# Performance work log

Hardware: AMD Instinct MI355X
Metric: run time of the kernel (lower is better)

The kernel has to match this reference:

```python
import jax, jax.numpy as jnp
import numpy as np

N, D, H, C = 4096, 4096, 256, 16
NNZ_ATTR, E, NNZ_JM, NNZ_JA = 262144, 131072, 400000, 80000


def setup_inputs() -> dict:
    key = jax.random.key(0)
    ks = jax.random.split(key, 8)
    return {
        "attr_row": jax.random.randint(ks[0], (NNZ_ATTR,), 0, N),
        "attr_col": jax.random.randint(ks[1], (NNZ_ATTR,), 0, D),
        "edge_idx": jax.random.randint(ks[2], (2, E), 0, N),
        "j_mask_idx": jax.random.randint(ks[3], (2, NNZ_JM), 0, N),
        "jaug_mask_idx": jax.random.randint(ks[4], (2, NNZ_JA), 0, N),
        "lin1_w": jax.random.normal(ks[5], (H, D), dtype=jnp.float32) * (1.0 / np.sqrt(D)),
        "lin2_w": jax.random.normal(ks[6], (C, H), dtype=jnp.float32) * (1.0 / np.sqrt(H)),
        "bias2": jax.random.normal(ks[7], (C,), dtype=jnp.float32) * 0.01,
        "n": N,
        "d": D,
    }


def _gcn_norm_dense(a, n):
    # add remaining self loops (binary adjacency -> set diagonal to 1)
    idx = jnp.arange(n)
    a = a.at[idx, idx].set(1.0)
    # PyG gcn_norm: deg = scatter_add(weight, col) = column sums
    deg = a.sum(axis=0)
    dinv = jnp.where(deg > 0, jax.lax.rsqrt(deg), 0.0)
    # out[i] = sum_j dinv[i]*dinv[j]*A[j,i]*x[j]  ->  An = Dinv @ A^T @ Dinv
    return (dinv[:, None] * a.T) * dinv[None, :]


def reference(attr_row, attr_col, edge_idx, j_mask_idx, jaug_mask_idx,
              lin1_w, lin2_w, bias2, n, d):
    # --- edge augmentation: (edges AND J_mask) OR JAug_mask ---
    a = jnp.zeros((n, n), jnp.float32).at[edge_idx[0], edge_idx[1]].set(1.0)
    jm = jnp.zeros((n, n), bool).at[j_mask_idx[0], j_mask_idx[1]].set(True)
    ja = jnp.zeros((n, n), bool).at[jaug_mask_idx[0], jaug_mask_idx[1]].set(True)
    a_aug = jnp.maximum(jnp.where(jm, a, 0.0), ja.astype(jnp.float32))

    # --- layer 1: spmm(sparse binary X, W1^T), gcn_norm, propagate (no bias) ---
    x = jnp.zeros((n, d), jnp.float32).at[attr_row, attr_col].add(1.0)
    h = x @ lin1_w.T                     # [n, H]
    an = _gcn_norm_dense(a_aug, n)       # [n, n] normalized adjacency
    h = jax.nn.relu(an @ h)              # propagate + relu
    # dropout is identity in eval mode

    # --- layer 2: standard GCNConv with bias ---
    h2 = h @ lin2_w.T                    # [n, C]
    out = an @ h2 + bias2
    return out
```

## Files before the change

kernel.cpp:

```cpp
#include <hip/hip_runtime.h>

#define N_      4096
#define D_      4096
#define H_      256
#define C_      16
#define NNZ_ATTR 262144
#define E_      131072
#define NNZ_JM  400000
#define NNZ_JA  80000
#define WORDS   128
#define ADJ_STRIDE 128
#define ASTR    128
#define NT      256

#define OFF_EBT  ((size_t)0)
#define OFF_ABT  ((size_t)(2u<<20))
#define OFF_CNT  ((size_t)(4u<<20))
#define OFF_DINV (OFF_CNT + (size_t)(16u<<10))
#define OFF_DEG  (OFF_CNT + (size_t)(32u<<10))
#define OFF_CCOL (OFF_CNT + (size_t)(48u<<10))
#define OFF_ADJ  (OFF_CCOL + (size_t)(2u<<20))
#define OFF_W1T  (OFF_ADJ + (size_t)(2u<<20))
#define OFF_H1   (OFF_W1T + (size_t)(4u<<20))
#define OFF_H2   (OFF_H1  + (size_t)(4u<<20))

#define ZERO_BYTES (OFF_CNT + (size_t)(16u<<10))
#define ZB_BLOCKS  1028

#define SB_ATTR  0
#define SB_EDGE  1024
#define SB_JA    1536
#define SB_DIAG  1849
#define SB_TR    1865
#define SB_TOTAL 2889

__global__ void k_zero(uint4* __restrict__ zp) {
    zp[(size_t)blockIdx.x * NT + threadIdx.x] = make_uint4(0u, 0u, 0u, 0u);
}

__global__ void k_scat1(const int* __restrict__ attr_row, const int* __restrict__ attr_col,
                        const int* __restrict__ edge, const int* __restrict__ jaug,
                        const float* __restrict__ w1,
                        unsigned* __restrict__ ebt, unsigned* __restrict__ abt,
                        unsigned* __restrict__ cnt, unsigned* __restrict__ ccol,
                        float* __restrict__ w1t) {
    __shared__ float tile[32][33];
    const int b = blockIdx.x, t = threadIdx.x;
    if (b < SB_EDGE) {
        int i = b * NT + t;
        int r = attr_row[i];
        unsigned pos = atomicAdd(&cnt[r], 1u);
        if (pos < ASTR) ccol[(size_t)r * ASTR + pos] = (unsigned)attr_col[i];
    } else if (b < SB_JA) {
        int j = (b - SB_EDGE) * NT + t;
        int p = edge[j], q = edge[E_ + j];
        atomicOr(&ebt[(size_t)q * WORDS + (p >> 5)], 1u << (p & 31));
    } else if (b < SB_DIAG) {
        int j = (b - SB_JA) * NT + t;
        if (j < NNZ_JA) {
            int p = jaug[j], q = jaug[NNZ_JA + j];
            atomicOr(&abt[(size_t)q * WORDS + (p >> 5)], 1u << (p & 31));
        }
    } else if (b < SB_TR) {
        int r = (b - SB_DIAG) * NT + t;
        atomicOr(&abt[(size_t)r * WORDS + (r >> 5)], 1u << (r & 31));
    } else {
        int bb = b - SB_TR;
        int gx = bb & 127, gy = bb >> 7;
        int tx = t & 31, ty = t >> 5;
        int col = gx * 32 + tx;
        #pragma unroll
        for (int j = 0; j < 4; ++j)
            tile[ty + j * 8][tx] = w1[(size_t)(gy * 32 + ty + j * 8) * D_ + col];
        __syncthreads();
        int ocol = gy * 32 + tx;
        #pragma unroll
        for (int j = 0; j < 4; ++j)
            w1t[(size_t)(gx * 32 + ty + j * 8) * H_ + ocol] = tile[tx][ty + j * 8];
    }
}

__global__ void k_scat2(const int* __restrict__ jmsk,
                        const unsigned* __restrict__ ebt, unsigned* __restrict__ abt) {
    int i = blockIdx.x * NT + threadIdx.x;
    if (i >= NNZ_JM) return;
    int p = jmsk[i], q = jmsk[NNZ_JM + i];
    size_t w = (size_t)q * WORDS + (p >> 5);
    if ((ebt[w] >> (p & 31)) & 1u)
        atomicOr(&abt[w], 1u << (p & 31));
}

__global__ void k_rowh1(const unsigned* __restrict__ abt, const unsigned* __restrict__ cnt,
                        const unsigned* __restrict__ ccol, const float* __restrict__ w1t,
                        float* __restrict__ dinv, int* __restrict__ deg,
                        int* __restrict__ adj, float* __restrict__ h1s) {
    __shared__ __align__(16) char smem[4640];
    unsigned* cols = (unsigned*)smem;
    float* part = (float*)(smem + 512);
    float* sdinv = (float*)(smem + 512 + 4096);
    const int b = blockIdx.x, t = threadIdx.x;
    int wv = t >> 6, lane = t & 63;
    int q = 4 * b + wv;
    {
        uint2 m2 = ((const uint2*)(abt + (size_t)q * WORDS))[lane];
        unsigned w0 = m2.x, w1b = m2.y;
        int c = __popc(w0) + __popc(w1b);
        int pre = c;
        #pragma unroll
        for (int d2 = 1; d2 < 64; d2 <<= 1) {
            int x = __shfl_up(pre, d2);
            if (lane >= d2) pre += x;
        }
        int excl = pre - c;
        int total = __shfl(pre, 63);
        if (lane == 0) {
            float dv = rsqrtf((float)total);
            dinv[q] = dv;
            sdinv[wv] = dv;
            deg[q] = total < ADJ_STRIDE ? total : ADJ_STRIDE;
        }
        unsigned idx = (unsigned)excl;
        int* arow = adj + (size_t)q * ADJ_STRIDE;
        int base0 = lane * 64;
        while (w0)  { int bp = __ffs(w0) - 1;  w0  &= w0 - 1;  if (idx < ADJ_STRIDE) arow[idx] = base0 + bp;      ++idx; }
        while (w1b) { int bp = __ffs(w1b) - 1; w1b &= w1b - 1; if (idx < ADJ_STRIDE) arow[idx] = base0 + 32 + bp; ++idx; }
    }
    __syncthreads();
    int g = t >> 6;
    for (int i = 0; i < 4; ++i) {
        int r = 4 * b + i;
        unsigned m = min(cnt[r], (unsigned)ASTR);
        if ((unsigned)t < m) cols[t] = ccol[(size_t)r * ASTR + t];
        __syncthreads();
        float4 acc = make_float4(0.f, 0.f, 0.f, 0.f);
        unsigned j = (unsigned)g;
        for (; j + 12 < m; j += 16) {
            unsigned c0 = cols[j], c1 = cols[j + 4], c2 = cols[j + 8], c3 = cols[j + 12];
            float4 v0 = *(const float4*)&w1t[(size_t)c0 * H_ + lane * 4];
            float4 v1 = *(const float4*)&w1t[(size_t)c1 * H_ + lane * 4];
            float4 v2 = *(const float4*)&w1t[(size_t)c2 * H_ + lane * 4];
            float4 v3 = *(const float4*)&w1t[(size_t)c3 * H_ + lane * 4];
            acc.x += v0.x + v1.x + v2.x + v3.x;
            acc.y += v0.y + v1.y + v2.y + v3.y;
            acc.z += v0.z + v1.z + v2.z + v3.z;
            acc.w += v0.w + v1.w + v2.w + v3.w;
        }
        for (; j < m; j += 4) {
            unsigned c0 = cols[j];
            float4 v0 = *(const float4*)&w1t[(size_t)c0 * H_ + lane * 4];
            acc.x += v0.x; acc.y += v0.y; acc.z += v0.z; acc.w += v0.w;
        }
        ((float4*)part)[g * 64 + lane] = acc;
        __syncthreads();
        int comp = t & 3, idx4 = t >> 2;
        float s0 = part[(0 * 64 + idx4) * 4 + comp];
        float s1 = part[(1 * 64 + idx4) * 4 + comp];
        float s2 = part[(2 * 64 + idx4) * 4 + comp];
        float s3 = part[(3 * 64 + idx4) * 4 + comp];
        h1s[(size_t)r * H_ + t] = (s0 + s1 + s2 + s3) * sdinv[i];
        __syncthreads();
    }
}

__global__ void k_prop1(const int* __restrict__ adj, const int* __restrict__ deg,
                        const float* __restrict__ dinv, const float* __restrict__ h1s,
                        const float* __restrict__ w2, float* __restrict__ h2s) {
    __shared__ __align__(16) char smem[2688];
    int* adj_s = (int*)smem;
    float* hrow = (float*)(smem + 512);
    float* partial = (float*)(smem + 512 + 1024);
    const int b = blockIdx.x, t = threadIdx.x;
    int c = t & 15, g = t >> 4;
    float w2r[16];
    #pragma unroll
    for (int kk = 0; kk < 16; ++kk) w2r[kk] = w2[(size_t)c * H_ + g * 16 + kk];
    for (int i = 0; i < 4; ++i) {
        int q = 4 * b + i;
        __syncthreads();
        if (t < ADJ_STRIDE) adj_s[t] = adj[(size_t)q * ADJ_STRIDE + t];
        __syncthreads();
        int dg = deg[q];
        float acc = 0.f;
        int j = 0;
        for (; j + 4 <= dg; j += 4) {
            int p0 = adj_s[j], p1 = adj_s[j + 1], p2 = adj_s[j + 2], p3 = adj_s[j + 3];
            acc += h1s[(size_t)p0 * H_ + t] + h1s[(size_t)p1 * H_ + t]
                 + h1s[(size_t)p2 * H_ + t] + h1s[(size_t)p3 * H_ + t];
        }
        for (; j < dg; ++j) acc += h1s[(size_t)adj_s[j] * H_ + t];
        float dq = dinv[q];
        hrow[t] = fmaxf(acc * dq, 0.f);
        __syncthreads();
        float part = 0.f;
        #pragma unroll
        for (int kk = 0; kk < 16; ++kk) part += hrow[g * 16 + kk] * w2r[kk];
        partial[g * 17 + c] = part;
        __syncthreads();
        if (t < 16) {
            float s = 0.f;
            #pragma unroll
            for (int g2 = 0; g2 < 16; ++g2) s += partial[g2 * 17 + t];
            h2s[(size_t)q * C_ + t] = s * dq;
        }
    }
}

__global__ void k_prop2(const int* __restrict__ adj, const int* __restrict__ deg,
                        const float* __restrict__ dinv, const float* __restrict__ h2s,
                        const float* __restrict__ bias, float* __restrict__ out) {
    const int b = blockIdx.x, t = threadIdx.x;
    int wv = t >> 6, lane = t & 63;
    int q = 4 * b + wv;
    int c = lane & 15, prt = lane >> 4;
    int dg = deg[q];
    const int* arow = adj + (size_t)q * ADJ_STRIDE;
    float acc = 0.f;
    for (int j = prt; j < dg; j += 4)
        acc += h2s[(size_t)arow[j] * C_ + c];
    acc += __shfl_down(acc, 32);
    acc += __shfl_down(acc, 16);
    if (lane < 16)
        out[(size_t)q * C_ + c] = dinv[q] * acc + bias[c];
}


extern "C" void kernel_launch(void* const* d_in, const int* in_sizes, int n_in,
                              void* d_out, int out_size, void* d_ws, size_t ws_size,
                              hipStream_t stream) {
    const int*   attr_row = (const int*)d_in[0];
    const int*   attr_col = (const int*)d_in[1];
    const int*   edge     = (const int*)d_in[2];
    const int*   jmsk     = (const int*)d_in[3];
    const int*   jaug     = (const int*)d_in[4];
    const float* w1       = (const float*)d_in[5];
    const float* w2       = (const float*)d_in[6];
    const float* bias2    = (const float*)d_in[7];
    float*       out      = (float*)d_out;

    char* ws = (char*)d_ws;
    unsigned* ebt  = (unsigned*)(ws + OFF_EBT);
    unsigned* abt  = (unsigned*)(ws + OFF_ABT);
    unsigned* cnt  = (unsigned*)(ws + OFF_CNT);
    float*    dinv = (float*)(ws + OFF_DINV);
    int*      deg  = (int*)(ws + OFF_DEG);
    unsigned* ccol = (unsigned*)(ws + OFF_CCOL);
    int*      adj  = (int*)(ws + OFF_ADJ);
    float*    w1t  = (float*)(ws + OFF_W1T);
    float*    h1s  = (float*)(ws + OFF_H1);
    float*    h2s  = (float*)(ws + OFF_H2);

    k_zero<<<ZB_BLOCKS, NT, 0, stream>>>((uint4*)d_ws);
    k_scat1<<<SB_TOTAL, NT, 0, stream>>>(attr_row, attr_col, edge, jaug, w1,
                                         ebt, abt, cnt, ccol, w1t);
    k_scat2<<<(NNZ_JM + NT - 1) / NT, NT, 0, stream>>>(jmsk, ebt, abt);
    k_rowh1<<<N_ / 4, NT, 0, stream>>>(abt, cnt, ccol, w1t, dinv, deg, adj, h1s);
    k_prop1<<<N_ / 4, NT, 0, stream>>>(adj, deg, dinv, h1s, w2, h2s);
    k_prop2<<<N_ / 4, NT, 0, stream>>>(adj, deg, dinv, h2s, bias2, out);
}
```

Measured before the change: 81.51 us.

## Store W1^T and H1 in fp16 and merge zeroing with weight transpose

```diff
diff --git a/kernel.cpp b/kernel.cpp
--- a/kernel.cpp
+++ b/kernel.cpp
@@ -13,43 +13,60 @@
 #define ASTR    128
 #define NT      256
 
+typedef _Float16 half8v __attribute__((ext_vector_type(8)));
+typedef _Float16 half2v __attribute__((ext_vector_type(2)));
+
 #define OFF_EBT  ((size_t)0)
 #define OFF_ABT  ((size_t)(2u<<20))
 #define OFF_CNT  ((size_t)(4u<<20))
-#define OFF_DINV (OFF_CNT + (size_t)(16u<<10))
-#define OFF_DEG  (OFF_CNT + (size_t)(32u<<10))
-#define OFF_CCOL (OFF_CNT + (size_t)(48u<<10))
+#define OFF_DINV (OFF_CNT + (size_t)(256u<<10))
+#define OFF_DEG  (OFF_DINV + (size_t)(16u<<10))
+#define OFF_CCOL (OFF_DEG + (size_t)(16u<<10))
 #define OFF_ADJ  (OFF_CCOL + (size_t)(2u<<20))
 #define OFF_W1T  (OFF_ADJ + (size_t)(2u<<20))
-#define OFF_H1   (OFF_W1T + (size_t)(4u<<20))
-#define OFF_H2   (OFF_H1  + (size_t)(4u<<20))
-
-#define ZERO_BYTES (OFF_CNT + (size_t)(16u<<10))
-#define ZB_BLOCKS  1028
-
-#define SB_ATTR  0
+#define OFF_H1   (OFF_W1T + (size_t)(2u<<20))
+#define OFF_H2   (OFF_H1  + (size_t)(2u<<20))
+
+#define ZERO_BYTES ((size_t)((4u<<20)+(256u<<10)))
+#define ZB_BLOCKS  1088
+#define TR_BLOCKS  1024
+
 #define SB_EDGE  1024
 #define SB_JA    1536
 #define SB_DIAG  1849
-#define SB_TR    1865
-#define SB_TOTAL 2889
-
-__global__ void k_zero(uint4* __restrict__ zp) {
-    zp[(size_t)blockIdx.x * NT + threadIdx.x] = make_uint4(0u, 0u, 0u, 0u);
+#define SB_TOTAL 1865
+
+__global__ void k_pre(const float* __restrict__ w1, _Float16* __restrict__ w1t,
+                      uint4* __restrict__ zp) {
+    __shared__ float tile[32][33];
+    int b = blockIdx.x, t = threadIdx.x;
+    if (b < ZB_BLOCKS) {
+        zp[(size_t)b * NT + t] = make_uint4(0u, 0u, 0u, 0u);
+    } else {
+        int bb = b - ZB_BLOCKS;
+        int gx = bb & 127, gy = bb >> 7;
+        int tx = t & 31, ty = t >> 5;
+        int col = gx * 32 + tx;
+        #pragma unroll
+        for (int j = 0; j < 4; ++j)
+            tile[ty + j * 8][tx] = w1[(size_t)(gy * 32 + ty + j * 8) * D_ + col];
+        __syncthreads();
+        int ocol = gy * 32 + tx;
+        #pragma unroll
+        for (int j = 0; j < 4; ++j)
+            w1t[(size_t)(gx * 32 + ty + j * 8) * H_ + ocol] = (_Float16)tile[tx][ty + j * 8];
+    }
 }
 
 __global__ void k_scat1(const int* __restrict__ attr_row, const int* __restrict__ attr_col,
                         const int* __restrict__ edge, const int* __restrict__ jaug,
-                        const float* __restrict__ w1,
                         unsigned* __restrict__ ebt, unsigned* __restrict__ abt,
-                        unsigned* __restrict__ cnt, unsigned* __restrict__ ccol,
-                        float* __restrict__ w1t) {
-    __shared__ float tile[32][33];
+                        unsigned* __restrict__ cnt, unsigned* __restrict__ ccol) {
     const int b = blockIdx.x, t = threadIdx.x;
     if (b < SB_EDGE) {
         int i = b * NT + t;
         int r = attr_row[i];
-        unsigned pos = atomicAdd(&cnt[r], 1u);
+        unsigned pos = atomicAdd(&cnt[r << 4], 1u);
         if (pos < ASTR) ccol[(size_t)r * ASTR + pos] = (unsigned)attr_col[i];
     } else if (b < SB_JA) {
         int j = (b - SB_EDGE) * NT + t;
@@ -61,22 +78,9 @@
             int p = jaug[j], q = jaug[NNZ_JA + j];
             atomicOr(&abt[(size_t)q * WORDS + (p >> 5)], 1u << (p & 31));
         }
-    } else if (b < SB_TR) {
+    } else {
         int r = (b - SB_DIAG) * NT + t;
         atomicOr(&abt[(size_t)r * WORDS + (r >> 5)], 1u << (r & 31));
-    } else {
-        int bb = b - SB_TR;
-        int gx = bb & 127, gy = bb >> 7;
-        int tx = t & 31, ty = t >> 5;
-        int col = gx * 32 + tx;
-        #pragma unroll
-        for (int j = 0; j < 4; ++j)
-            tile[ty + j * 8][tx] = w1[(size_t)(gy * 32 + ty + j * 8) * D_ + col];
-        __syncthreads();
-        int ocol = gy * 32 + tx;
-        #pragma unroll
-        for (int j = 0; j < 4; ++j)
-            w1t[(size_t)(gx * 32 + ty + j * 8) * H_ + ocol] = tile[tx][ty + j * 8];
     }
 }
 
@@ -91,13 +95,12 @@
 }
 
 __global__ void k_rowh1(const unsigned* __restrict__ abt, const unsigned* __restrict__ cnt,
-                        const unsigned* __restrict__ ccol, const float* __restrict__ w1t,
+                        const unsigned* __restrict__ ccol, const _Float16* __restrict__ w1t,
                         float* __restrict__ dinv, int* __restrict__ deg,
-                        int* __restrict__ adj, float* __restrict__ h1s) {
-    __shared__ __align__(16) char smem[4640];
-    unsigned* cols = (unsigned*)smem;
-    float* part = (float*)(smem + 512);
-    float* sdinv = (float*)(smem + 512 + 4096);
+                        int* __restrict__ adj, _Float16* __restrict__ h1s) {
+    __shared__ unsigned cols[128];
+    __shared__ float part[4][2][32][8];
+    __shared__ float sdinv[4];
     const int b = blockIdx.x, t = threadIdx.x;
     int wv = t >> 6, lane = t & 63;
     int q = 4 * b + wv;
@@ -126,80 +129,89 @@
         while (w1b) { int bp = __ffs(w1b) - 1; w1b &= w1b - 1; if (idx < ADJ_STRIDE) arow[idx] = base0 + 32 + bp; ++idx; }
     }
     __syncthreads();
-    int g = t >> 6;
+    int g = t >> 6, hw = (t >> 5) & 1, l32 = t & 31;
     for (int i = 0; i < 4; ++i) {
         int r = 4 * b + i;
-        unsigned m = min(cnt[r], (unsigned)ASTR);
-        if ((unsigned)t < m) cols[t] = ccol[(size_t)r * ASTR + t];
-        __syncthreads();
-        float4 acc = make_float4(0.f, 0.f, 0.f, 0.f);
-        unsigned j = (unsigned)g;
-        for (; j + 12 < m; j += 16) {
-            unsigned c0 = cols[j], c1 = cols[j + 4], c2 = cols[j + 8], c3 = cols[j + 12];
-            float4 v0 = *(const float4*)&w1t[(size_t)c0 * H_ + lane * 4];
-            float4 v1 = *(const float4*)&w1t[(size_t)c1 * H_ + lane * 4];
-            float4 v2 = *(const float4*)&w1t[(size_t)c2 * H_ + lane * 4];
-            float4 v3 = *(const float4*)&w1t[(size_t)c3 * H_ + lane * 4];
-            acc.x += v0.x + v1.x + v2.x + v3.x;
-            acc.y += v0.y + v1.y + v2.y + v3.y;
-            acc.z += v0.z + v1.z + v2.z + v3.z;
-            acc.w += v0.w + v1.w + v2.w + v3.w;
-        }
-        for (; j < m; j += 4) {
-            unsigned c0 = cols[j];
-            float4 v0 = *(const float4*)&w1t[(size_t)c0 * H_ + lane * 4];
-            acc.x += v0.x; acc.y += v0.y; acc.z += v0.z; acc.w += v0.w;
-        }
-        ((float4*)part)[g * 64 + lane] = acc;
-        __syncthreads();
-        int comp = t & 3, idx4 = t >> 2;
-        float s0 = part[(0 * 64 + idx4) * 4 + comp];
-        float s1 = part[(1 * 64 + idx4) * 4 + comp];
-        float s2 = part[(2 * 64 + idx4) * 4 + comp];
-        float s3 = part[(3 * 64 + idx4) * 4 + comp];
-        h1s[(size_t)r * H_ + t] = (s0 + s1 + s2 + s3) * sdinv[i];
+        int m = (int)min(cnt[r << 4], (unsigned)ASTR);
+        if (t < m) cols[t] = ccol[(size_t)r * ASTR + t];
+        __syncthreads();
+        float acc[8];
+        #pragma unroll
+        for (int e = 0; e < 8; ++e) acc[e] = 0.f;
+        int sub = (g << 1) + hw;
+        for (int j = 0; j < m; j += 8) {
+            int jc = j + sub;
+            if (jc < m) {
+                unsigned c = cols[jc];
+                half8v v = *(const half8v*)(w1t + (size_t)c * H_ + l32 * 8);
+                #pragma unroll
+                for (int e = 0; e < 8; ++e) acc[e] += (float)v[e];
+            }
+        }
+        #pragma unroll
+        for (int e = 0; e < 8; ++e) part[g][hw][l32][e] = acc[e];
+        __syncthreads();
+        int l = t >> 3, e = t & 7;
+        float s = 0.f;
+        #pragma unroll
+        for (int gg = 0; gg < 4; ++gg) {
+            s += part[gg][0][l][e];
+            s += part[gg][1][l][e];
+        }
+        h1s[(size_t)r * H_ + t] = (_Float16)(s * sdinv[i]);
         __syncthreads();
     }
 }
 
 __global__ void k_prop1(const int* __restrict__ adj, const int* __restrict__ deg,
-                        const float* __restrict__ dinv, const float* __restrict__ h1s,
+                        const float* __restrict__ dinv, const _Float16* __restrict__ h1s,
                         const float* __restrict__ w2, float* __restrict__ h2s) {
-    __shared__ __align__(16) char smem[2688];
-    int* adj_s = (int*)smem;
-    float* hrow = (float*)(smem + 512);
-    float* partial = (float*)(smem + 512 + 1024);
-    const int b = blockIdx.x, t = threadIdx.x;
-    int c = t & 15, g = t >> 4;
+    __shared__ int adj_s[128];
+    __shared__ float partial2[2][256];
+    __shared__ float hrow[256];
+    __shared__ float partial[16][17];
+    const int b = blockIdx.x, t = threadIdx.x;
+    int g2 = t >> 7, tt = t & 127;
+    int c = t & 15, gg = t >> 4;
     float w2r[16];
     #pragma unroll
-    for (int kk = 0; kk < 16; ++kk) w2r[kk] = w2[(size_t)c * H_ + g * 16 + kk];
+    for (int kk = 0; kk < 16; ++kk) w2r[kk] = w2[(size_t)c * H_ + gg * 16 + kk];
     for (int i = 0; i < 4; ++i) {
         int q = 4 * b + i;
         __syncthreads();
         if (t < ADJ_STRIDE) adj_s[t] = adj[(size_t)q * ADJ_STRIDE + t];
         __syncthreads();
         int dg = deg[q];
-        float acc = 0.f;
-        int j = 0;
-        for (; j + 4 <= dg; j += 4) {
-            int p0 = adj_s[j], p1 = adj_s[j + 1], p2 = adj_s[j + 2], p3 = adj_s[j + 3];
-            acc += h1s[(size_t)p0 * H_ + t] + h1s[(size_t)p1 * H_ + t]
-                 + h1s[(size_t)p2 * H_ + t] + h1s[(size_t)p3 * H_ + t];
-        }
-        for (; j < dg; ++j) acc += h1s[(size_t)adj_s[j] * H_ + t];
+        float ax = 0.f, ay = 0.f;
+        int j = g2;
+        for (; j + 2 < dg; j += 4) {
+            int p0 = adj_s[j], p1 = adj_s[j + 2];
+            half2v v0 = *(const half2v*)(h1s + (size_t)p0 * H_ + tt * 2);
+            half2v v1 = *(const half2v*)(h1s + (size_t)p1 * H_ + tt * 2);
+            ax += (float)v0[0] + (float)v1[0];
+            ay += (float)v0[1] + (float)v1[1];
+        }
+        for (; j < dg; j += 2) {
+            int p0 = adj_s[j];
+            half2v v0 = *(const half2v*)(h1s + (size_t)p0 * H_ + tt * 2);
+            ax += (float)v0[0];
+            ay += (float)v0[1];
+        }
+        partial2[g2][2 * tt]     = ax;
+        partial2[g2][2 * tt + 1] = ay;
+        __syncthreads();
         float dq = dinv[q];
-        hrow[t] = fmaxf(acc * dq, 0.f);
-        __syncthreads();
-        float part = 0.f;
-        #pragma unroll
-        for (int kk = 0; kk < 16; ++kk) part += hrow[g * 16 + kk] * w2r[kk];
-        partial[g * 17 + c] = part;
+        hrow[t] = fmaxf((partial2[0][t] + partial2[1][t]) * dq, 0.f);
+        __syncthreads();
+        float p = 0.f;
+        #pragma unroll
+        for (int kk = 0; kk < 16; ++kk) p += hrow[gg * 16 + kk] * w2r[kk];
+        partial[gg][c] = p;
         __syncthreads();
         if (t < 16) {
             float s = 0.f;
             #pragma unroll
-            for (int g2 = 0; g2 < 16; ++g2) s += partial[g2 * 17 + t];
+            for (int g3 = 0; g3 < 16; ++g3) s += partial[g3][t];
             h2s[(size_t)q * C_ + t] = s * dq;
         }
     }
@@ -238,20 +250,20 @@
     float*       out      = (float*)d_out;
 
     char* ws = (char*)d_ws;
-    unsigned* ebt  = (unsigned*)(ws + OFF_EBT);
-    unsigned* abt  = (unsigned*)(ws + OFF_ABT);
-    unsigned* cnt  = (unsigned*)(ws + OFF_CNT);
-    float*    dinv = (float*)(ws + OFF_DINV);
-    int*      deg  = (int*)(ws + OFF_DEG);
-    unsigned* ccol = (unsigned*)(ws + OFF_CCOL);
-    int*      adj  = (int*)(ws + OFF_ADJ);
-    float*    w1t  = (float*)(ws + OFF_W1T);
-    float*    h1s  = (float*)(ws + OFF_H1);
-    float*    h2s  = (float*)(ws + OFF_H2);
-
-    k_zero<<<ZB_BLOCKS, NT, 0, stream>>>((uint4*)d_ws);
-    k_scat1<<<SB_TOTAL, NT, 0, stream>>>(attr_row, attr_col, edge, jaug, w1,
-                                         ebt, abt, cnt, ccol, w1t);
+    unsigned*  ebt  = (unsigned*)(ws + OFF_EBT);
+    unsigned*  abt  = (unsigned*)(ws + OFF_ABT);
+    unsigned*  cnt  = (unsigned*)(ws + OFF_CNT);
+    float*     dinv = (float*)(ws + OFF_DINV);
+    int*       deg  = (int*)(ws + OFF_DEG);
+    unsigned*  ccol = (unsigned*)(ws + OFF_CCOL);
+    int*       adj  = (int*)(ws + OFF_ADJ);
+    _Float16*  w1t  = (_Float16*)(ws + OFF_W1T);
+    _Float16*  h1s  = (_Float16*)(ws + OFF_H1);
+    float*     h2s  = (float*)(ws + OFF_H2);
+
+    k_pre<<<ZB_BLOCKS + TR_BLOCKS, NT, 0, stream>>>(w1, w1t, (uint4*)d_ws);
+    k_scat1<<<SB_TOTAL, NT, 0, stream>>>(attr_row, attr_col, edge, jaug,
+                                         ebt, abt, cnt, ccol);
     k_scat2<<<(NNZ_JM + NT - 1) / NT, NT, 0, stream>>>(jmsk, ebt, abt);
     k_rowh1<<<N_ / 4, NT, 0, stream>>>(abt, cnt, ccol, w1t, dinv, deg, adj, h1s);
     k_prop1<<<N_ / 4, NT, 0, stream>>>(adj, deg, dinv, h1s, w2, h2s);
```

Result: faster. 75.46 us (median of 2 runs) (-7.4%).
